# Kernel optimization log

Measured on AMD Instinct MI355X. Metric: run time of the kernel, lower is better.

## Reference

```python
import jax, jax.numpy as jnp
import numpy as np

N = 100000       # nodes
E = 1600000      # edges (avg degree 16)
F_IN = 128
F_HID = 64
F_OUT = 40
K = 10
ALPHA = 0.1


def setup_inputs() -> dict:
    key = jax.random.key(0)
    k1, k2, k3, k4, k5, k6 = jax.random.split(key, 6)
    x = jax.random.normal(k1, (N, F_IN), dtype=jnp.float32)
    edge_index = jax.random.randint(k2, (2, E), 0, N, dtype=jnp.int32)
    # Linear params (Kaiming-uniform-ish scale)
    W1 = jax.random.normal(k3, (F_IN, F_HID), dtype=jnp.float32) / np.sqrt(F_IN)
    b1 = jax.random.normal(k4, (F_HID,), dtype=jnp.float32) * 0.01
    W2 = jax.random.normal(k5, (F_HID, F_OUT), dtype=jnp.float32) / np.sqrt(F_HID)
    b2 = jax.random.normal(k6, (F_OUT,), dtype=jnp.float32) * 0.01
    return {"x": x, "edge_index": edge_index, "W1": W1, "b1": b1, "W2": W2, "b2": b2}


def _gcn_norm(edge_index, dtype):
    # add self loops, symmetric normalization D^{-1/2} (A+I) D^{-1/2}
    loops = jnp.arange(N, dtype=edge_index.dtype)
    src = jnp.concatenate([edge_index[0], loops])
    dst = jnp.concatenate([edge_index[1], loops])
    deg = jax.ops.segment_sum(jnp.ones_like(src, dtype=dtype), dst, num_segments=N)
    dinv = jnp.where(deg > 0, jax.lax.rsqrt(deg), 0.0).astype(dtype)
    norm = dinv[src] * dinv[dst]  # [E + N]
    return src, dst, norm


def _appnp(x, src, dst, norm):
    h = x  # teleport target
    def step(xc, _):
        agg = jax.ops.segment_sum(xc[src] * norm[:, None], dst, num_segments=N)
        return (1.0 - ALPHA) * agg + ALPHA * h, None
    out, _ = jax.lax.scan(step, x, None, length=K)
    return out


def reference(x, edge_index, W1, b1, W2, b2):
    src, dst, norm = _gcn_norm(edge_index, x.dtype)
    # layer 1: Linear -> relu -> (dropout p=0) -> APPNP
    h = jax.nn.relu(x @ W1 + b1)
    h = _appnp(h, src, dst, norm)
    # layer 2: Linear -> relu -> APPNP
    h = jax.nn.relu(h @ W2 + b2)
    h = _appnp(h, src, dst, norm)
    return jax.nn.log_softmax(h, axis=1)
```

## Files before the change

### kernel.cpp

```cpp
#include <hip/hip_runtime.h>
#include <hip/hip_fp16.h>
#include <hip/hip_fp8.h>
#include <hip/hip_cooperative_groups.h>

namespace cg = cooperative_groups;

namespace {
constexpr int NN = 100000;
constexpr int NE = 1600000;
constexpr int FIN = 128, FHID = 64, FOUT = 40;
constexpr float ALPHA = 0.1f;
constexpr int SLOTS = 64;
constexpr int SB = 40;
constexpr int ECHUNK = 200000;
constexpr int GPB = 102;
constexpr int NCH = (NN + GPB - 1) / GPB;

typedef int v4i __attribute__((ext_vector_type(4)));
typedef unsigned int v2u __attribute__((ext_vector_type(2)));
typedef unsigned int v4u __attribute__((ext_vector_type(4)));
typedef float v2f __attribute__((ext_vector_type(2)));
typedef float v4f __attribute__((ext_vector_type(4)));
typedef _Float16 half8 __attribute__((ext_vector_type(8)));

#if __has_builtin(__builtin_amdgcn_cvt_pk_f32_fp8) && __has_builtin(__builtin_amdgcn_cvt_pk_fp8_f32)
#define HW_FP8 1
#else
#define HW_FP8 0
#endif

__device__ __forceinline__ ushort f2h(float v) {
  union { __half h; ushort u; } cv;
  cv.h = __float2half_rn(v);
  return cv.u;
}

__device__ __forceinline__ void acc8_fp8(v2u w, float* a) {
#if HW_FP8
  v2f p0 = __builtin_amdgcn_cvt_pk_f32_fp8((int)w.x, false);
  v2f p1 = __builtin_amdgcn_cvt_pk_f32_fp8((int)w.x, true);
  v2f p2 = __builtin_amdgcn_cvt_pk_f32_fp8((int)w.y, false);
  v2f p3 = __builtin_amdgcn_cvt_pk_f32_fp8((int)w.y, true);
  a[0] += p0.x; a[1] += p0.y; a[2] += p1.x; a[3] += p1.y;
  a[4] += p2.x; a[5] += p2.y; a[6] += p3.x; a[7] += p3.y;
#else
  union { v2u w; unsigned char b[8]; } cv;
  cv.w = w;
#pragma unroll
  for (int k = 0; k < 8; k++) {
    __hip_fp8_e4m3 h;
    h.__x = cv.b[k];
    a[k] += (float)h;
  }
#endif
}

__device__ __forceinline__ v2u enc8_fp8(const float* o) {
#if HW_FP8
  int d0 = __builtin_amdgcn_cvt_pk_fp8_f32(o[0], o[1], 0, false);
  d0 = __builtin_amdgcn_cvt_pk_fp8_f32(o[2], o[3], d0, true);
  int d1 = __builtin_amdgcn_cvt_pk_fp8_f32(o[4], o[5], 0, false);
  d1 = __builtin_amdgcn_cvt_pk_fp8_f32(o[6], o[7], d1, true);
  v2u r;
  r.x = (unsigned int)d0;
  r.y = (unsigned int)d1;
  return r;
#else
  union { v2u w; unsigned char b[8]; } cv;
#pragma unroll
  for (int k = 0; k < 8; k++) {
    __hip_fp8_e4m3 h(o[k]);
    cv.b[k] = h.__x;
  }
  return cv.w;
#endif
}

__device__ __forceinline__ unsigned int enc4_fp8(float a, float b, float c, float d) {
#if HW_FP8
  int d0 = __builtin_amdgcn_cvt_pk_fp8_f32(a, b, 0, false);
  d0 = __builtin_amdgcn_cvt_pk_fp8_f32(c, d, d0, true);
  return (unsigned int)d0;
#else
  union { unsigned char b4[4]; unsigned int u; } cv;
  __hip_fp8_e4m3 h0(a), h1(b), h2(c), h3(d);
  cv.b4[0] = h0.__x; cv.b4[1] = h1.__x; cv.b4[2] = h2.__x; cv.b4[3] = h3.__x;
  return cv.u;
#endif
}

__global__ void k_zero(int* cnt) {
  int i = blockIdx.x * 256 + threadIdx.x;
  if (i < NN) cnt[i] = 0;
}

__global__ void k_fill_ell(const int* __restrict__ src, const int* __restrict__ dst,
                           int* __restrict__ cnt, int* __restrict__ ell, int ebase) {
  int e = ebase + blockIdx.x * 256 + threadIdx.x;
  if (e >= ebase + ECHUNK || e >= NE) return;
  int s = src[e], d = dst[e];
  int p = atomicAdd(&cnt[d], 1);
  if (p < SLOTS) ell[(size_t)p * NN + d] = s;
}

__global__ void k_dinv(const int* __restrict__ cnt, float2* __restrict__ dd) {
  int i = blockIdx.x * 256 + threadIdx.x;
  if (i < NN) {
    float di = rsqrtf((float)(cnt[i] + 1));
    dd[i] = make_float2(di, 0.9f * di * di);
  }
}

__global__ __launch_bounds__(256, 3) void k_mlp(const float* __restrict__ x,
                                                const float* __restrict__ W1,
                                                const float* __restrict__ b1,
                                                const float* __restrict__ W2,
                                                const float2* __restrict__ dd,
                                                float* __restrict__ h2x,
                                                ushort* __restrict__ u0,
                                                unsigned char* __restrict__ uq) {
  __shared__ _Float16 w1t[64 * 136];
  __shared__ _Float16 w2t[48 * 72];
  __shared__ unsigned int ht[4 * 16 * 36];

  int tid = threadIdx.x;
  for (int i = tid; i < 2048; i += 256) {
    float4 v = ((const float4*)W1)[i];
    int k = i >> 4;
    int c0 = (i & 15) * 4;
    w1t[(c0 + 0) * 136 + k] = (_Float16)v.x;
    w1t[(c0 + 1) * 136 + k] = (_Float16)v.y;
    w1t[(c0 + 2) * 136 + k] = (_Float16)v.z;
    w1t[(c0 + 3) * 136 + k] = (_Float16)v.w;
  }
  for (int i = tid; i < 2560; i += 256) {
    int k = i / 40, c = i - k * 40;
    w2t[c * 72 + k] = (_Float16)W2[i];
  }
  for (int i = tid; i < 576; i += 256) w2t[2880 + i] = (_Float16)0.f;
  __syncthreads();

  int wid = tid >> 6, lane = tid & 63;
  int g = lane >> 4, n = lane & 15;
  int node = blockIdx.x * 64 + wid * 16 + n;
  int nodeL = node < NN ? node : NN - 1;
  const float* xr = x + (size_t)nodeL * FIN;

  v4f acc1[4] = {};
#pragma unroll
  for (int kk = 0; kk < 4; kk++) {
    const float4* xp = (const float4*)(xr + kk * 32 + g * 8);
    float4 xa = xp[0], xb = xp[1];
    half8 bx;
    bx[0] = (_Float16)xa.x; bx[1] = (_Float16)xa.y;
    bx[2] = (_Float16)xa.z; bx[3] = (_Float16)xa.w;
    bx[4] = (_Float16)xb.x; bx[5] = (_Float16)xb.y;
    bx[6] = (_Float16)xb.z; bx[7] = (_Float16)xb.w;
#pragma unroll
    for (int mt = 0; mt < 4; mt++) {
      half8 af = *(const half8*)(w1t + (mt * 16 + n) * 136 + kk * 32 + g * 8);
      acc1[mt] = __builtin_amdgcn_mfma_f32_16x16x32_f16(af, bx, acc1[mt], 0, 0, 0);
    }
  }

  unsigned int* hw = ht + wid * 576 + n * 36;
#pragma unroll
  for (int mt = 0; mt < 4; mt++) {
    float4 bb = *(const float4*)(b1 + mt * 16 + g * 4);
    union { _Float16 h[4]; uint2 u; } pk;
    pk.h[0] = (_Float16)fmaxf(acc1[mt][0] + bb.x, 0.f);
    pk.h[1] = (_Float16)fmaxf(acc1[mt][1] + bb.y, 0.f);
    pk.h[2] = (_Float16)fmaxf(acc1[mt][2] + bb.z, 0.f);
    pk.h[3] = (_Float16)fmaxf(acc1[mt][3] + bb.w, 0.f);
    *(uint2*)(hw + mt * 8 + g * 2) = pk.u;
  }

  v4f acc2[3] = {};
#pragma unroll
  for (int kk = 0; kk < 2; kk++) {
    half8 bh = *(const half8*)((const _Float16*)(hw + kk * 16 + g * 4));
#pragma unroll
    for (int mt2 = 0; mt2 < 3; mt2++) {
      half8 af = *(const half8*)(w2t + (mt2 * 16 + n) * 72 + kk * 32 + g * 8);
      acc2[mt2] = __builtin_amdgcn_mfma_f32_16x16x32_f16(af, bh, acc2[mt2], 0, 0, 0);
    }
  }

  if (node < NN) {
    float di = dd[node].x;
#pragma unroll
    for (int mt2 = 0; mt2 < 3; mt2++) {
      int c0 = mt2 * 16 + g * 4;
      if (c0 < FOUT) {
        float y0 = acc2[mt2][0], y1 = acc2[mt2][1];
        float y2 = acc2[mt2][2], y3 = acc2[mt2][3];
        *(float4*)(h2x + (size_t)node * FOUT + c0) = make_float4(y0, y1, y2, y3);
        float u0v = di * y0, u1v = di * y1, u2v = di * y2, u3v = di * y3;
        union { ushort s[4]; uint2 q; } hq;
        hq.s[0] = f2h(u0v); hq.s[1] = f2h(u1v);
        hq.s[2] = f2h(u2v); hq.s[3] = f2h(u3v);
        *(uint2*)(u0 + (size_t)node * FOUT + c0) = hq.q;
        *(unsigned int*)(uq + (size_t)node * SB + c0) = enc4_fp8(u0v, u1v, u2v, u3v);
      }
    }
  }
}

__global__ __launch_bounds__(512, 8) void k_appnp_all(
    const int* __restrict__ cnt, const int* __restrict__ ell,
    const float2* __restrict__ dd, ushort* __restrict__ u0,
    const float* __restrict__ b2, const float* __restrict__ h2x,
    ushort* __restrict__ zh,
    unsigned char* __restrict__ q0, unsigned char* __restrict__ qA,
    unsigned char* __restrict__ qB) {
  __shared__ int sidx[GPB][SLOTS + 1];
  __shared__ int sdeg[GPB];

  int tid = threadIdx.x;
  int base = blockIdx.x * GPB;
  if (tid < GPB) {
    int n = base + tid;
    int d = (n < NN) ? cnt[n] : 0;
    sdeg[tid] = d > SLOTS ? SLOTS : d;
  }
  __syncthreads();
  for (int i = tid; i < GPB * SLOTS; i += 512) {
    int p = i / GPB, n = i - p * GPB;
    int node = base + n;
    if (node < NN && p < sdeg[n]) sidx[n][p] = ell[(size_t)p * NN + node];
  }
  __syncthreads();

  int nd = tid / 5, ch = tid - nd * 5;
  int node = base + nd;
  bool act = (nd < GPB) && (node < NN);
  int deg = act ? sdeg[nd] : 0;
  float di = 0.f, c9 = 0.f;
  if (act) {
    float2 d2 = dd[node];
    di = d2.x;
    c9 = d2.y;
  }
  union { v4u q; __half h[8]; } t0;
  if (act) t0.q = *(const v4u*)(u0 + (size_t)node * FOUT + ch * 8);

  cg::grid_group grid = cg::this_grid();

  auto gather = [&](const unsigned char* u, float* a) {
    const unsigned char* ub = u + ch * 8;
#pragma unroll
    for (int k = 0; k < 8; k++) a[k] = 0.f;
    acc8_fp8(*(const v2u*)(ub + (size_t)node * SB), a);
    int j = 0;
    for (; j + 8 <= deg; j += 8) {
      v2u w[8];
#pragma unroll
      for (int k = 0; k < 8; k++)
        w[k] = *(const v2u*)(ub + (size_t)sidx[nd][j + k] * SB);
#pragma unroll
      for (int k = 0; k < 8; k++) acc8_fp8(w[k], a);
    }
    for (; j < deg; j++)
      acc8_fp8(*(const v2u*)(ub + (size_t)sidx[nd][j] * SB), a);
  };

  const unsigned char* cu = q0;
  for (int it = 0; it < 9; it++) {
    unsigned char* nx = (it & 1) ? qB : qA;
    if (act) {
      float a[8];
      gather(cu, a);
      float o[8];
#pragma unroll
      for (int k = 0; k < 8; k++) o[k] = c9 * a[k] + ALPHA * __half2float(t0.h[k]);
      *(v2u*)(nx + (size_t)node * SB + ch * 8) = enc8_fp8(o);
    }
    __threadfence();
    grid.sync();
    cu = nx;
  }

  union { v4u q; __half h[8]; } ghr;
  if (act) {
    float a[8];
    gather(cu, a);
    v4f h0 = *(const v4f*)(h2x + (size_t)node * FOUT + ch * 8);
    v4f h1 = *(const v4f*)(h2x + (size_t)node * FOUT + ch * 8 + 4);
    const float* bb = b2 + ch * 8;
    float hx[8] = {h0.x, h0.y, h0.z, h0.w, h1.x, h1.y, h1.z, h1.w};
    float t9 = 0.9f * di;
    float g[8], ug[8];
#pragma unroll
    for (int k = 0; k < 8; k++) {
      float z = t9 * a[k] + ALPHA * hx[k] + bb[k];
      g[k] = fmaxf(z, 0.f);
      ug[k] = di * g[k];
    }
#pragma unroll
    for (int k = 0; k < 8; k++) {
      ghr.h[k] = __float2half_rn(g[k]);
      t0.h[k] = __float2half_rn(ug[k]);
    }
    *(v2u*)(q0 + (size_t)node * SB + ch * 8) = enc8_fp8(ug);
  }
  __threadfence();
  grid.sync();

  cu = q0;
  for (int it = 0; it < 9; it++) {
    unsigned char* nx = (it & 1) ? qB : qA;
    if (act) {
      float a[8];
      gather(cu, a);
      float o[8];
#pragma unroll
      for (int k = 0; k < 8; k++) o[k] = c9 * a[k] + ALPHA * __half2float(t0.h[k]);
      *(v2u*)(nx + (size_t)node * SB + ch * 8) = enc8_fp8(o);
    }
    __threadfence();
    grid.sync();
    cu = nx;
  }

  if (act) {
    float a[8];
    gather(cu, a);
    float t9 = 0.9f * di;
    union { v4u u4; __half h[8]; } cv;
#pragma unroll
    for (int k = 0; k < 8; k++)
      cv.h[k] = __float2half_rn(t9 * a[k] + ALPHA * __half2float(ghr.h[k]));
    *(v4u*)(zh + (size_t)node * FOUT + ch * 8) = cv.u4;
  }
}

__device__ __forceinline__ void gather_pm(const int* __restrict__ ell,
                                          const unsigned char* __restrict__ u,
                                          int node, int ch, int deg, float* a) {
#pragma unroll
  for (int k = 0; k < 8; k++) a[k] = 0.f;
  const unsigned char* ub = u + ch * 8;
  v2u ws = *(const v2u*)(ub + (size_t)node * SB);
  int q[8], qn[8];
#pragma unroll
  for (int k = 0; k < 8; k++) q[k] = ell[(size_t)k * NN + node];
  acc8_fp8(ws, a);
  int j = 0;
  for (; j + 8 <= deg; j += 8) {
#pragma unroll
    for (int k = 0; k < 8; k++) {
      int pl = j + 8 + k;
      pl = pl > SLOTS - 1 ? SLOTS - 1 : pl;
      qn[k] = ell[(size_t)pl * NN + node];
    }
    v2u w[8];
#pragma unroll
    for (int k = 0; k < 8; k++) w[k] = *(const v2u*)(ub + (size_t)q[k] * SB);
#pragma unroll
    for (int k = 0; k < 8; k++) acc8_fp8(w[k], a);
#pragma unroll
    for (int k = 0; k < 8; k++) q[k] = qn[k];
  }
  int rr = deg - j;
#pragma unroll
  for (int k = 0; k < 7; k++) {
    if (k < rr) acc8_fp8(*(const v2u*)(ub + (size_t)q[k] * SB), a);
  }
}

#define APPNP_HDR(cntp)                            \
  int tid = threadIdx.x;                           \
  int nd = tid / 5, ch = tid - nd * 5;             \
  int node = blockIdx.x * 64 + nd;                 \
  if (node >= NN) return;                          \
  int deg = (cntp)[node];                          \
  deg = deg > SLOTS ? SLOTS : deg;

__device__ __forceinline__ void store_h8(ushort* p, const float* v) {
  union { v4u u; __half h[8]; } cv;
#pragma unroll
  for (int k = 0; k < 8; k++) cv.h[k] = __float2half_rn(v[k]);
  *(v4u*)p = cv.u;
}

__global__ __launch_bounds__(320, 6) void k_mid(const int* __restrict__ cnt,
                                                const int* __restrict__ ell,
                                                const float2* __restrict__ dd,
                                                const ushort* __restrict__ u0,
                                                const unsigned char* __restrict__ u,
                                                unsigned char* __restrict__ un) {
  APPNP_HDR(cnt)
  union { v4u q; __half h[8]; } t0;
  t0.q = *(const v4u*)(u0 + (size_t)node * FOUT + ch * 8);
  float c9 = dd[node].y;
  float a[8];
  gather_pm(ell, u, node, ch, deg, a);
  float o[8];
#pragma unroll
  for (int k = 0; k < 8; k++) o[k] = c9 * a[k] + ALPHA * __half2float(t0.h[k]);
  v2u st = enc8_fp8(o);
  *(v2u*)(un + (size_t)node * SB + ch * 8) = st;
}

__global__ __launch_bounds__(320, 6) void k_final1(const int* __restrict__ cnt,
                                                   const int* __restrict__ ell,
                                                   const float2* __restrict__ dd,
                                                   const float* __restrict__ b2,
                                                   const float* __restrict__ h2x,
                                                   const unsigned char* __restrict__ u,
                                                   ushort* __restrict__ gh,
                                                   ushort* __restrict__ u0n,
                                                   unsigned char* __restrict__ uqn) {
  APPNP_HDR(cnt)
  float di = dd[node].x;
  v4f h0 = __builtin_nontemporal_load((const v4f*)(h2x + (size_t)node * FOUT + ch * 8));
  v4f h1 = __builtin_nontemporal_load((const v4f*)(h2x + (size_t)node * FOUT + ch * 8 + 4));
  const float* bb = b2 + ch * 8;
  float a[8];
  gather_pm(ell, u, node, ch, deg, a);
  float t9 = 0.9f * di;
  float hx[8] = {h0.x, h0.y, h0.z, h0.w, h1.x, h1.y, h1.z, h1.w};
  float g[8], ug[8];
#pragma unroll
  for (int k = 0; k < 8; k++) {
    float z = t9 * a[k] + ALPHA * hx[k] + bb[k];
    g[k] = fmaxf(z, 0.f);
    ug[k] = di * g[k];
  }
  store_h8(gh + (size_t)node * FOUT + ch * 8, g);
  store_h8(u0n + (size_t)node * FOUT + ch * 8, ug);
  v2u st = enc8_fp8(ug);
  *(v2u*)(uqn + (size_t)node * SB + ch * 8) = st;
}

__global__ __launch_bounds__(320, 6) void k_final2(const int* __restrict__ cnt,
                                                   const int* __restrict__ ell,
                                                   const float2* __restrict__ dd,
                                                   const ushort* __restrict__ gh,
                                                   const unsigned char* __restrict__ u,
                                                   ushort* __restrict__ zh) {
  APPNP_HDR(cnt)
  union { v4u q; __half h[8]; } hv;
  hv.q = *(const v4u*)(gh + (size_t)node * FOUT + ch * 8);
  float t9 = 0.9f * dd[node].x;
  float a[8];
  gather_pm(ell, u, node, ch, deg, a);
  float o[8];
#pragma unroll
  for (int k = 0; k < 8; k++) o[k] = t9 * a[k] + ALPHA * __half2float(hv.h[k]);
  store_h8(zh + (size_t)node * FOUT + ch * 8, o);
}

__global__ void k_logsoftmax(const ushort* __restrict__ in, float* __restrict__ out) {
  int i = blockIdx.x * 256 + threadIdx.x;
  if (i >= NN) return;
  union { v4u q; __half h[8]; } v[5];
  const v4u* r = (const v4u*)(in + (size_t)i * FOUT);
  float f[40];
  float m = -1e30f;
#pragma unroll
  for (int j = 0; j < 5; j++) {
    v[j].q = r[j];
#pragma unroll
    for (int k = 0; k < 8; k++) {
      f[j * 8 + k] = __half2float(v[j].h[k]);
      m = fmaxf(m, f[j * 8 + k]);
    }
  }
  float sum = 0.f;
#pragma unroll
  for (int j = 0; j < 40; j++) sum += expf(f[j] - m);
  float lse = m + logf(sum);
  float4* o = (float4*)(out + (size_t)i * FOUT);
#pragma unroll
  for (int j = 0; j < 10; j++) {
    float4 w = {f[j * 4] - lse, f[j * 4 + 1] - lse, f[j * 4 + 2] - lse, f[j * 4 + 3] - lse};
    o[j] = w;
  }
}

}

extern "C" void kernel_launch(void* const* d_in, const int* in_sizes, int n_in,
                              void* d_out, int out_size, void* d_ws, size_t ws_size,
                              hipStream_t stream) {
  const float* x = (const float*)d_in[0];
  const int* ei = (const int*)d_in[1];
  const int* src = ei;
  const int* dst = ei + NE;
  const float* W1 = (const float*)d_in[2];
  const float* b1 = (const float*)d_in[3];
  const float* W2 = (const float*)d_in[4];
  const float* b2 = (const float*)d_in[5];
  float* out = (float*)d_out;

  char* ws = (char*)d_ws;
  size_t off = 0;
  auto alloc = [&](size_t bytes) -> void* {
    void* p = ws + off;
    off += (bytes + 255) & ~(size_t)255;
    return p;
  };
  int* cnt          = (int*)alloc((size_t)NN * 4);
  float2* dd        = (float2*)alloc((size_t)NN * 8);
  int* ell          = (int*)alloc((size_t)NN * SLOTS * 4);
  float* h2x        = (float*)alloc((size_t)NN * FOUT * 4);
  ushort* u0h       = (ushort*)alloc((size_t)NN * FOUT * 2);
  ushort* gh        = (ushort*)alloc((size_t)NN * FOUT * 2);
  ushort* zh        = (ushort*)alloc((size_t)NN * FOUT * 2);
  unsigned char* q0 = (unsigned char*)alloc((size_t)NN * SB);
  unsigned char* qA = (unsigned char*)alloc((size_t)NN * SB);
  unsigned char* qB = (unsigned char*)alloc((size_t)NN * SB);

  k_zero<<<(NN + 255) / 256, 256, 0, stream>>>(cnt);
  for (int c = 0; c < NE / ECHUNK; c++)
    k_fill_ell<<<(ECHUNK + 255) / 256, 256, 0, stream>>>(src, dst, cnt, ell, c * ECHUNK);
  k_dinv<<<(NN + 255) / 256, 256, 0, stream>>>(cnt, dd);

  k_mlp<<<(NN + 63) / 64, 256, 0, stream>>>(x, W1, b1, W2, dd, h2x, u0h, q0);

  static int coopTotal = -1;
  if (coopTotal < 0) {
    int nb = 0;
    hipOccupancyMaxActiveBlocksPerMultiprocessor(&nb, k_appnp_all, 512, 0);
    coopTotal = nb * 256;
  }
  if (coopTotal >= NCH) {
    void* kargs[] = {(void*)&cnt, (void*)&ell, (void*)&dd,  (void*)&u0h,
                     (void*)&b2,  (void*)&h2x, (void*)&zh,  (void*)&q0,
                     (void*)&qA,  (void*)&qB};
    hipLaunchCooperativeKernel((void*)k_appnp_all, dim3(NCH), dim3(512), kargs, 0, stream);
  } else {
    int agrid = (NN + 63) / 64;
    const unsigned char* cu = q0;
    for (int it = 0; it < 9; it++) {
      unsigned char* nx = (it & 1) ? qB : qA;
      k_mid<<<agrid, 320, 0, stream>>>(cnt, ell, dd, u0h, cu, nx);
      cu = nx;
    }
    k_final1<<<agrid, 320, 0, stream>>>(cnt, ell, dd, b2, h2x, cu, gh, u0h, q0);
    cu = q0;
    for (int it = 0; it < 9; it++) {
      unsigned char* nx = (it & 1) ? qB : qA;
      k_mid<<<agrid, 320, 0, stream>>>(cnt, ell, dd, u0h, cu, nx);
      cu = nx;
    }
    k_final2<<<agrid, 320, 0, stream>>>(cnt, ell, dd, gh, cu, zh);
  }

  k_logsoftmax<<<(NN + 255) / 256, 256, 0, stream>>>(zh, out);
}
```

Measured before the change: 639.9 us.

## Pad FP8 feature rows to 48 bytes and gather 16 features per thread

Pads each node's FP8 feature row from 40 to 48 bytes so three threads per node can each load 16 bytes with one 128-bit gather, replacing five threads doing 8-byte loads. More nodes are handled per block (170 instead of 102), and the b2 bias is staged in shared memory. The aim is to halve the number of gather instructions per edge and raise bytes per load in the latency-bound sparse propagation. The cost is 20% more bytes per row, padding lanes that carry zeros, more registers per thread (occupancy hint lowered to 6), and reads past the 40-column end of h2x/u0, which are covered by extra allocation slack.

Result: slower. 664.4 us (+3.8%).

```diff
diff --git a/kernel.cpp b/kernel.cpp
--- a/kernel.cpp
+++ b/kernel.cpp
@@ -11,9 +11,9 @@
 constexpr int FIN = 128, FHID = 64, FOUT = 40;
 constexpr float ALPHA = 0.1f;
 constexpr int SLOTS = 64;
-constexpr int SB = 40;
+constexpr int SB = 48;
 constexpr int ECHUNK = 200000;
-constexpr int GPB = 102;
+constexpr int GPB = 170;
 constexpr int NCH = (NN + GPB - 1) / GPB;
 
 typedef int v4i __attribute__((ext_vector_type(4)));
@@ -53,6 +53,14 @@
     a[k] += (float)h;
   }
 #endif
+}
+
+__device__ __forceinline__ void acc16_fp8(v4u w, float* a) {
+  v2u lo, hi;
+  lo.x = w.x; lo.y = w.y;
+  hi.x = w.z; hi.y = w.w;
+  acc8_fp8(lo, a);
+  acc8_fp8(hi, a + 8);
 }
 
 __device__ __forceinline__ v2u enc8_fp8(const float* o) {
@@ -201,12 +209,14 @@
         hq.s[2] = f2h(u2v); hq.s[3] = f2h(u3v);
         *(uint2*)(u0 + (size_t)node * FOUT + c0) = hq.q;
         *(unsigned int*)(uq + (size_t)node * SB + c0) = enc4_fp8(u0v, u1v, u2v, u3v);
+        if (c0 == 32)
+          *(uint2*)(uq + (size_t)node * SB + 40) = make_uint2(0u, 0u);
       }
     }
   }
 }
 
-__global__ __launch_bounds__(512, 8) void k_appnp_all(
+__global__ __launch_bounds__(512, 6) void k_appnp_all(
     const int* __restrict__ cnt, const int* __restrict__ ell,
     const float2* __restrict__ dd, ushort* __restrict__ u0,
     const float* __restrict__ b2, const float* __restrict__ h2x,
@@ -215,6 +225,7 @@
     unsigned char* __restrict__ qB) {
   __shared__ int sidx[GPB][SLOTS + 1];
   __shared__ int sdeg[GPB];
+  __shared__ float sb2[48];
 
   int tid = threadIdx.x;
   int base = blockIdx.x * GPB;
@@ -223,6 +234,7 @@
     int d = (n < NN) ? cnt[n] : 0;
     sdeg[tid] = d > SLOTS ? SLOTS : d;
   }
+  if (tid < 48) sb2[tid] = (tid < FOUT) ? b2[tid] : 0.f;
   __syncthreads();
   for (int i = tid; i < GPB * SLOTS; i += 512) {
     int p = i / GPB, n = i - p * GPB;
@@ -231,77 +243,96 @@
   }
   __syncthreads();
 
-  int nd = tid / 5, ch = tid - nd * 5;
+  int nd = tid / 3, r = tid - nd * 3;
   int node = base + nd;
   bool act = (nd < GPB) && (node < NN);
-  int deg = act ? sdeg[nd] : 0;
+  int deg = 0;
   float di = 0.f, c9 = 0.f;
   if (act) {
+    deg = sdeg[nd];
     float2 d2 = dd[node];
     di = d2.x;
     c9 = d2.y;
   }
-  union { v4u q; __half h[8]; } t0;
-  if (act) t0.q = *(const v4u*)(u0 + (size_t)node * FOUT + ch * 8);
+  union { v4u q[2]; __half h[16]; } t0;
+  if (act) {
+    t0.q[0] = *(const v4u*)(u0 + (size_t)node * FOUT + r * 16);
+    t0.q[1] = *(const v4u*)(u0 + (size_t)node * FOUT + r * 16 + 8);
+  }
 
   cg::grid_group grid = cg::this_grid();
 
   auto gather = [&](const unsigned char* u, float* a) {
-    const unsigned char* ub = u + ch * 8;
-#pragma unroll
-    for (int k = 0; k < 8; k++) a[k] = 0.f;
-    acc8_fp8(*(const v2u*)(ub + (size_t)node * SB), a);
+    const unsigned char* ub = u + r * 16;
+#pragma unroll
+    for (int k = 0; k < 16; k++) a[k] = 0.f;
+    acc16_fp8(*(const v4u*)(ub + (size_t)node * SB), a);
     int j = 0;
-    for (; j + 8 <= deg; j += 8) {
-      v2u w[8];
-#pragma unroll
-      for (int k = 0; k < 8; k++)
-        w[k] = *(const v2u*)(ub + (size_t)sidx[nd][j + k] * SB);
-#pragma unroll
-      for (int k = 0; k < 8; k++) acc8_fp8(w[k], a);
+    for (; j + 4 <= deg; j += 4) {
+      v4u w0 = *(const v4u*)(ub + (size_t)sidx[nd][j + 0] * SB);
+      v4u w1 = *(const v4u*)(ub + (size_t)sidx[nd][j + 1] * SB);
+      v4u w2 = *(const v4u*)(ub + (size_t)sidx[nd][j + 2] * SB);
+      v4u w3 = *(const v4u*)(ub + (size_t)sidx[nd][j + 3] * SB);
+      acc16_fp8(w0, a);
+      acc16_fp8(w1, a);
+      acc16_fp8(w2, a);
+      acc16_fp8(w3, a);
     }
     for (; j < deg; j++)
-      acc8_fp8(*(const v2u*)(ub + (size_t)sidx[nd][j] * SB), a);
+      acc16_fp8(*(const v4u*)(ub + (size_t)sidx[nd][j] * SB), a);
   };
 
   const unsigned char* cu = q0;
   for (int it = 0; it < 9; it++) {
     unsigned char* nx = (it & 1) ? qB : qA;
     if (act) {
-      float a[8];
+      float a[16];
       gather(cu, a);
-      float o[8];
-#pragma unroll
-      for (int k = 0; k < 8; k++) o[k] = c9 * a[k] + ALPHA * __half2float(t0.h[k]);
-      *(v2u*)(nx + (size_t)node * SB + ch * 8) = enc8_fp8(o);
+      unsigned int e[4];
+#pragma unroll
+      for (int h = 0; h < 2; h++) {
+        float o[8];
+#pragma unroll
+        for (int k = 0; k < 8; k++)
+          o[k] = c9 * a[h * 8 + k] + ALPHA * __half2float(t0.h[h * 8 + k]);
+        v2u p = enc8_fp8(o);
+        e[2 * h] = p.x;
+        e[2 * h + 1] = p.y;
+      }
+      v4u st; st.x = e[0]; st.y = e[1]; st.z = e[2]; st.w = e[3];
+      *(v4u*)(nx + (size_t)node * SB + r * 16) = st;
     }
     __threadfence();
     grid.sync();
     cu = nx;
   }
 
-  union { v4u q; __half h[8]; } ghr;
+  union { v4u q[2]; __half h[16]; } ghr;
   if (act) {
-    float a[8];
+    float a[16];
     gather(cu, a);
-    v4f h0 = *(const v4f*)(h2x + (size_t)node * FOUT + ch * 8);
-    v4f h1 = *(const v4f*)(h2x + (size_t)node * FOUT + ch * 8 + 4);
-    const float* bb = b2 + ch * 8;
-    float hx[8] = {h0.x, h0.y, h0.z, h0.w, h1.x, h1.y, h1.z, h1.w};
     float t9 = 0.9f * di;
-    float g[8], ug[8];
-#pragma unroll
-    for (int k = 0; k < 8; k++) {
-      float z = t9 * a[k] + ALPHA * hx[k] + bb[k];
-      g[k] = fmaxf(z, 0.f);
-      ug[k] = di * g[k];
-    }
-#pragma unroll
-    for (int k = 0; k < 8; k++) {
-      ghr.h[k] = __float2half_rn(g[k]);
-      t0.h[k] = __float2half_rn(ug[k]);
-    }
-    *(v2u*)(q0 + (size_t)node * SB + ch * 8) = enc8_fp8(ug);
+    unsigned int e[4];
+#pragma unroll
+    for (int h = 0; h < 2; h++) {
+      v4f h0 = *(const v4f*)(h2x + (size_t)node * FOUT + r * 16 + h * 8);
+      v4f h1 = *(const v4f*)(h2x + (size_t)node * FOUT + r * 16 + h * 8 + 4);
+      float hx[8] = {h0.x, h0.y, h0.z, h0.w, h1.x, h1.y, h1.z, h1.w};
+      float ug[8];
+#pragma unroll
+      for (int k = 0; k < 8; k++) {
+        float z = t9 * a[h * 8 + k] + ALPHA * hx[k] + sb2[r * 16 + h * 8 + k];
+        float g = fmaxf(z, 0.f);
+        ug[k] = di * g;
+        ghr.h[h * 8 + k] = __float2half_rn(g);
+        t0.h[h * 8 + k] = __float2half_rn(ug[k]);
+      }
+      v2u p = enc8_fp8(ug);
+      e[2 * h] = p.x;
+      e[2 * h + 1] = p.y;
+    }
+    v4u st; st.x = e[0]; st.y = e[1]; st.z = e[2]; st.w = e[3];
+    *(v4u*)(q0 + (size_t)node * SB + r * 16) = st;
   }
   __threadfence();
   grid.sync();
@@ -310,12 +341,21 @@
   for (int it = 0; it < 9; it++) {
     unsigned char* nx = (it & 1) ? qB : qA;
     if (act) {
-      float a[8];
+      float a[16];
       gather(cu, a);
-      float o[8];
-#pragma unroll
-      for (int k = 0; k < 8; k++) o[k] = c9 * a[k] + ALPHA * __half2float(t0.h[k]);
-      *(v2u*)(nx + (size_t)node * SB + ch * 8) = enc8_fp8(o);
+      unsigned int e[4];
+#pragma unroll
+      for (int h = 0; h < 2; h++) {
+        float o[8];
+#pragma unroll
+        for (int k = 0; k < 8; k++)
+          o[k] = c9 * a[h * 8 + k] + ALPHA * __half2float(t0.h[h * 8 + k]);
+        v2u p = enc8_fp8(o);
+        e[2 * h] = p.x;
+        e[2 * h + 1] = p.y;
+      }
+      v4u st; st.x = e[0]; st.y = e[1]; st.z = e[2]; st.w = e[3];
+      *(v4u*)(nx + (size_t)node * SB + r * 16) = st;
     }
     __threadfence();
     grid.sync();
@@ -323,14 +363,19 @@
   }
 
   if (act) {
-    float a[8];
+    float a[16];
     gather(cu, a);
     float t9 = 0.9f * di;
-    union { v4u u4; __half h[8]; } cv;
-#pragma unroll
-    for (int k = 0; k < 8; k++)
+    union { v4u q[2]; __half h[16]; } cv;
+#pragma unroll
+    for (int k = 0; k < 16; k++)
       cv.h[k] = __float2half_rn(t9 * a[k] + ALPHA * __half2float(ghr.h[k]));
-    *(v4u*)(zh + (size_t)node * FOUT + ch * 8) = cv.u4;
+    if (r < 2) {
+      *(v4u*)(zh + (size_t)node * FOUT + r * 16) = cv.q[0];
+      *(v4u*)(zh + (size_t)node * FOUT + r * 16 + 8) = cv.q[1];
+    } else {
+      *(v4u*)(zh + (size_t)node * FOUT + 32) = cv.q[0];
+    }
   }
 }
 
@@ -504,8 +549,8 @@
   int* cnt          = (int*)alloc((size_t)NN * 4);
   float2* dd        = (float2*)alloc((size_t)NN * 8);
   int* ell          = (int*)alloc((size_t)NN * SLOTS * 4);
-  float* h2x        = (float*)alloc((size_t)NN * FOUT * 4);
-  ushort* u0h       = (ushort*)alloc((size_t)NN * FOUT * 2);
+  float* h2x        = (float*)alloc((size_t)NN * FOUT * 4 + 256);
+  ushort* u0h       = (ushort*)alloc((size_t)NN * FOUT * 2 + 256);
   ushort* gh        = (ushort*)alloc((size_t)NN * FOUT * 2);
   ushort* zh        = (ushort*)alloc((size_t)NN * FOUT * 2);
   unsigned char* q0 = (unsigned char*)alloc((size_t)NN * SB);
```
